# Optimization experiments

Hardware: AMD Instinct MI355X
Metric: run time of the kernel (lower is better)

## Reference

```python
import jax, jax.numpy as jnp
import numpy as np

EPS = 1e-15

def gcn_sparse(x, row, col, ew, W, b, n):
    # PyG GCNConv: h = x@W; add self-loops (weight 1); sym-normalize; aggregate at col (target); + bias
    h = x @ W
    loop = jnp.arange(n)
    r = jnp.concatenate([row, loop])
    c = jnp.concatenate([col, loop])
    w = jnp.concatenate([ew, jnp.ones((n,), x.dtype)])
    deg = jax.ops.segment_sum(w, c, num_segments=n)
    dinv = jnp.where(deg > 0, deg ** -0.5, 0.0)
    norm = dinv[r] * w * dinv[c]
    out = jax.ops.segment_sum(norm[:, None] * h[r], c, num_segments=n)
    return out + b

def gcn_dense(x, adj, W, b):
    # Dense equivalent of dense_to_sparse + GCNConv: existing nonzero self-loops keep their
    # weight, zero-diagonal nodes get a self-loop of weight 1 (add_remaining_self_loops).
    diag = jnp.diagonal(adj)
    adj_h = adj + jnp.diag(jnp.where(diag == 0, 1.0, 0.0).astype(adj.dtype))
    deg = adj_h.sum(axis=0)  # degree at target (col) nodes
    dinv = jnp.where(deg > 0, deg ** -0.5, 0.0)
    a_norm = dinv[:, None] * adj_h * dinv[None, :]  # norm_ij = d_i^-1/2 a_ij d_j^-1/2
    return a_norm.T @ (x @ W) + b  # out_j = sum_i norm_ij h_i

def diff_pool(x, adj, s, mask=None):
    s = jax.nn.softmax(s, axis=-1)
    if mask is not None:
        x = x * mask[:, None]
        s = s * mask[:, None]
    out = s.T @ x                      # [C, F]
    out_adj = s.T @ (adj @ s)          # [C, C]
    link = jnp.linalg.norm(adj - s @ s.T) / adj.size
    ent = jnp.mean(jnp.sum(-s * jnp.log(s + EPS), axis=-1))
    return out, out_adj, link, ent

def setup_inputs() -> dict:
    N, E, F, H, C1, C2, NC = 8192, 262144, 128, 128, 1024, 128, 16
    key = jax.random.key(0)
    ks = jax.random.split(key, 16)
    x0 = jax.random.normal(ks[0], (N, F), dtype=jnp.float32)
    edge_index = jax.random.randint(ks[1], (2, E), 0, N, dtype=jnp.int32)
    edge_weight = jax.random.uniform(ks[2], (E,), dtype=jnp.float32)
    adj = jnp.zeros((N, N), jnp.float32).at[edge_index[0], edge_index[1]].add(edge_weight)
    mask = jnp.ones((N,), jnp.float32)
    g = lambda k, i, o: jax.random.normal(k, (i, o), dtype=jnp.float32) * (1.0 / np.sqrt(i))
    return {
        'x0': x0, 'edge_index': edge_index, 'edge_weight': edge_weight,
        'adj': adj, 'mask': mask,
        'W0_in': g(ks[3], F, H),      'b0_in': jnp.zeros((H,)),
        'Wp1':   g(ks[4], H, C1),     'bp1':   jnp.zeros((C1,)),
        'W1_in': g(ks[5], H, H),      'b1_in': jnp.zeros((H,)),
        'Wp2':   g(ks[6], H, C2),     'bp2':   jnp.zeros((C2,)),
        'W2_in': g(ks[7], H, H),      'b2_in': jnp.zeros((H,)),
        'W1_out': g(ks[8], 2 * H, H), 'b1_out': jnp.zeros((H,)),
        'W0_out': g(ks[9], 2 * H, NC), 'b0_out': jnp.zeros((NC,)),
    }

def reference(x0, edge_index, edge_weight, adj, mask,
              W0_in, b0_in, Wp1, bp1, W1_in, b1_in, Wp2, bp2,
              W2_in, b2_in, W1_out, b1_out, W0_out, b0_out):
    n = x0.shape[0]
    row, col = edge_index[0], edge_index[1]
    x0_ = jax.nn.relu(gcn_sparse(x0, row, col, edge_weight, W0_in, b0_in, n))
    s1 = jax.nn.relu(gcn_sparse(x0_, row, col, edge_weight, Wp1, bp1, n))
    x1, adj1, l1, e1 = diff_pool(x0_, adj, s1, mask)
    x1_ = jax.nn.relu(gcn_dense(x1, adj1, W1_in, b1_in))
    s2 = jax.nn.relu(gcn_dense(x1_, adj1, Wp2, bp2))
    x2, adj2, l2, e2 = diff_pool(x1_, adj1, s2)
    x2_out = jax.nn.relu(gcn_dense(x2, adj2, W2_in, b2_in))
    x2_out_up = s2 @ x2_out  # unpool with pre-softmax relu s2, as in source
    x1_out = jax.nn.relu(gcn_dense(jnp.concatenate([x1_, x2_out_up], axis=1), adj1, W1_out, b1_out))
    x1_out_up = s1 @ x1_out
    x0_out = jax.nn.relu(gcn_sparse(jnp.concatenate([x0_, x1_out_up], axis=1), row, col, edge_weight, W0_out, b0_out, n))
    prediction = jax.nn.log_softmax(x0_out, axis=1)
    edge_loss = l1 + e1 + l2 + e2
    return prediction, s1, edge_loss, adj1
```

## Files before the change

### kernel.cpp

```cpp
#include <hip/hip_runtime.h>
#include <math.h>


#define N_NODES 8192
#define N_EDGES 262144

typedef __attribute__((ext_vector_type(8))) short short8;
typedef __attribute__((ext_vector_type(4))) float floatx4;

#define OFF_DEG     0
#define OFF_CNTC    8192
#define OFF_CNTR    16384
#define OFF_SCAL    24576
#define ZERO_FLOATS 24592
#define OFF_COLPTR  24592
#define OFF_ROWPTR  32785
#define OFF_CURC    40978
#define OFF_CURR    49170
#define OFF_COLR    57362
#define OFF_COLN    319506
#define OFF_ROWC    581650
#define OFF_ROWW    843794
#define OFF_DINV    1105938
#define OFF_X0      1114144
// ... 3 lines not shown
#define OFF_ADJ1B   (OFF_S+524288)
#define OFF_HAT     (OFF_S+1048576)
#define OFF_HBT     (OFF_S+1114112)
#define OFF_HCATT   (OFF_S+1179648)
#define OFF_S2ST    (OFF_S+1245184)
#define OFF_X0T     7405600
#define OFF_X0B     7929888
#define A2          8454176
#define OFF_X1      (A2+0)
#define OFF_Y16     (A2+131072)
#define OFF_X1_     (A2+262144)
#define OFF_S2      (A2+524288)
#define OFF_S2S     (A2+655360)
#define OFF_U       (A2+786432)
#define OFF_X2      (A2+917504)
#define OFF_ADJ2    (A2+933888)
#define OFF_HC      (A2+950272)
#define OFF_X2_     (A2+966656)
#define OFF_Z2      (A2+999424)
#define OFF_X1O     (A2+1261568)
#define OFF_P16     (A2+1392640)
#define OFF_DEG1    OFF_P16
#define OFF_DIAGV   (OFF_P16+1024)
#define OFF_DI1     (A2+1654784)
#define OFF_DF1     (A2+1655808)
#define OFF_DI2     (A2+1656832)
#define OFF_DF2     (A2+1656960)
#define OFF_ST      10111264
#define OFF_TBF     14305568
#define OFF_WP1T    OFF_TBF
#define OFF_PT      OFF_TBF
#define OFF_TT2     32131360

#define OUT_PRED 0
#define OUT_S1   131072
#define OUT_LOSS 8519680
#define OUT_ADJ1 8519681

__device__ __forceinline__ unsigned short f2bf(float f) {
    union { float f; unsigned u; } v; v.f = f;
    unsigned r = (v.u + 0x7FFF + ((v.u >> 16) & 1)) >> 16;
    return (unsigned short)r;
}
__device__ __forceinline__ float bf2f(unsigned short b) {
    union { unsigned u; float f; } v; v.u = (unsigned)b << 16; return v.f;
}
__device__ __forceinline__ void gl_lds16(const unsigned short* g, unsigned short* l) {
    __builtin_amdgcn_global_load_lds(
        (const __attribute__((address_space(1))) void*)g,
        (__attribute__((address_space(3))) void*)l, 16, 0, 0);
}


__global__ void k_hist(const int* __restrict__ row, const int* __restrict__ col,
// ... 287 lines not shown
            float a0 = As[ty * 2][kk], a1 = As[ty * 2 + 1][kk];
            float b0 = Bs[kk][tx * 2], b1 = Bs[kk][tx * 2 + 1];
            acc[0][0] += a0 * b0; acc[0][1] += a0 * b1;
            acc[1][0] += a1 * b0; acc[1][1] += a1 * b1;
        }
        __syncthreads();
    }
    if (op == 2) {
        float ss = acc[0][0] * acc[0][0] + acc[0][1] * acc[0][1]
                 + acc[1][0] * acc[1][0] + acc[1][1] * acc[1][1];
        red[tid] = ss; __syncthreads();
        for (int s = 128; s > 0; s >>= 1) { if (tid < s) red[tid] += red[tid + s]; __syncthreads(); }
        if (tid == 0) atomicAdd(ss_acc, red[0]);
        return;
    }
    float* C = (op == 0) ? C0 : C1;
    #pragma unroll
    for (int i = 0; i < 2; ++i)
        #pragma unroll
        for (int j = 0; j < 2; ++j)
            C[(size_t)(m0 + ty * 2 + i) * N + n0 + tx * 2 + j] = acc[i][j];
}

__global__ __launch_bounds__(256) void k_gemm_n16(const float* __restrict__ A, const float* __restrict__ B,
        float* __restrict__ C, int M, int K, int accum) {
    __shared__ float As[16][64];
    __shared__ float Bs[64][16];
    int tid = threadIdx.x;
    int r = tid >> 4, c = tid & 15;
    int m0 = blockIdx.x * 16;
    float acc = 0.f;
    for (int k0 = 0; k0 < K; k0 += 64) {
        #pragma unroll
        for (int l = 0; l < 4; ++l) {
            int idx = tid + 256 * l;
            int rr = idx >> 6, cc = idx & 63;
            As[rr][cc] = A[(size_t)(m0 + rr) * K + k0 + cc];
            int kk = idx >> 4, c2 = idx & 15;
            Bs[kk][c2] = B[(size_t)(k0 + kk) * 16 + c2];
        }
        __syncthreads();
        #pragma unroll 16
        for (int kk = 0; kk < 64; ++kk) acc += As[r][kk] * Bs[kk][c];
        __syncthreads();
    }
    float* p = &C[(size_t)(m0 + r) * 16 + c];
    if (accum) acc += *p;
    *p = acc;
}

__global__ __launch_bounds__(256) void k_gemm_n16_dual(
        const float* __restrict__ A0, int K0, const float* __restrict__ B0,
        const float* __restrict__ A1, int K1, const float* __restrict__ B1,
        float* __restrict__ C, int M) {
    __shared__ float As[16][64];
    __shared__ float Bs[64][16];
    int tid = threadIdx.x;
    int r = tid >> 4, c = tid & 15;
    int m0 = blockIdx.x * 16;
    float acc = 0.f;
    for (int src = 0; src < 2; ++src) {
        const float* A = src ? A1 : A0;
        const float* B = src ? B1 : B0;
        int K = src ? K1 : K0;
        for (int k0 = 0; k0 < K; k0 += 64) {
            #pragma unroll
            for (int l = 0; l < 4; ++l) {
                int idx = tid + 256 * l;
                int rr = idx >> 6, cc = idx & 63;
                As[rr][cc] = A[(size_t)(m0 + rr) * K + k0 + cc];
                int kk = idx >> 4, c2 = idx & 15;
                Bs[kk][c2] = B[(size_t)(k0 + kk) * 16 + c2];
            }
            __syncthreads();
            #pragma unroll 16
            for (int kk = 0; kk < 64; ++kk) acc += As[r][kk] * Bs[kk][c];
            __syncthreads();
        }
    }
    C[(size_t)(m0 + r) * 16 + c] = acc;
}


__global__ __launch_bounds__(256) void gemm_tn_bf16_tiles(
        const unsigned short* __restrict__ ST_,
        const unsigned short* __restrict__ TT_,
        const unsigned short* __restrict__ X0T_,
        float* __restrict__ P, int K) {
    __shared__ __align__(16) unsigned short As[128 * 64];
    __shared__ __align__(16) unsigned short Bs[128 * 64];
    int tid = threadIdx.x;
    int wave = tid >> 6, lane = tid & 63;
    int wm = wave >> 1, wn = wave & 1;
    int tile = blockIdx.x;
    int m, n; const unsigned short* B;
    if (tile < 64)       { m = tile >> 3; n = tile & 7; B = TT_; }
    else if (tile < 100) { int p = tile - 64; int ti = 0;
                           while (p >= 8 - ti) { p -= 8 - ti; ++ti; }
                           m = ti; n = ti + p; B = ST_; }
    else                 { m = tile - 100; n = 0; B = X0T_; }
    int m0 = m * 128, n0 = n * 128;
    int kchunk = K / gridDim.y;
    int k0 = blockIdx.y * kchunk;
    float* Pz = P + ((size_t)blockIdx.y * 108 + tile) * 16384;
    floatx4 acc[4][4] = {};
    int q = lane >> 4, lm = lane & 15;
    int lrow = lane >> 3, lcol = (lane & 7) * 8;
    for (int kt = 0; kt < kchunk; kt += 64) {
        int gk0 = k0 + kt;
        #pragma unroll
        for (int p = 0; p < 4; ++p) {
            int rbase = wave * 32 + p * 8;
            int row = rbase + lrow;
            int scol = lcol ^ ((row & 7) * 8);
            gl_lds16(&ST_[(size_t)(m0 + row) * K + gk0 + scol], &As[rbase * 64]);
            gl_lds16(&B[(size_t)(n0 + row) * K + gk0 + scol], &Bs[rbase * 64]);
        }
        __syncthreads();
        #pragma unroll
        for (int ks = 0; ks < 64; ks += 32) {
            short8 af[4], bf[4];
            int kk = ks + q * 8;
            #pragma unroll
            for (int i = 0; i < 4; ++i) {
                int ml = wm * 64 + i * 16 + lm;
                af[i] = *(const short8*)(&As[ml * 64 + (kk ^ ((ml & 7) * 8))]);
                int nl = wn * 64 + i * 16 + lm;
                bf[i] = *(const short8*)(&Bs[nl * 64 + (kk ^ ((nl & 7) * 8))]);
            }
            #pragma unroll
            for (int i = 0; i < 4; ++i)
                #pragma unroll
                for (int j = 0; j < 4; ++j)
                    acc[i][j] = __builtin_amdgcn_mfma_f32_16x16x32_bf16(af[i], bf[j], acc[i][j], 0, 0, 0);
        }
        __syncthreads();
    }
    for (int i = 0; i < 4; ++i) {
        int lr = wm * 64 + i * 16 + q * 4;
        for (int j = 0; j < 4; ++j) {
            int lc = wn * 64 + j * 16 + lm;
            #pragma unroll
            for (int r = 0; r < 4; ++r)
                Pz[(size_t)(lr + r) * 128 + lc] = acc[i][j][r];
        }
    }
}

__global__ __launch_bounds__(256) void k_reduce_tiles(
        const float* __restrict__ P,
        float* __restrict__ adj1o, unsigned short* __restrict__ adj1b,
        float* __restrict__ x1, float* __restrict__ deg1, float* __restrict__ diagv,
        float* __restrict__ scal) {
    __shared__ float colsum[128];
    __shared__ float red[256];
    int tile = blockIdx.y, half = blockIdx.x, tid = threadIdx.x;
    if (tid < 128) colsum[tid] = 0.f;
    __syncthreads();
    int m, n, kind;
    if (tile < 64)       { kind = 0; m = tile >> 3; n = tile & 7; }
    else if (tile < 100) { kind = 1; int p = tile - 64; int ti = 0;
                           while (p >= 8 - ti) { p -= 8 - ti; ++ti; }
                           m = ti; n = ti + p; }
    else                 { kind = 2; m = tile - 100; n = 0; }
    const float* Pt = P + (size_t)tile * 16384 + half * 8192;
    const size_t zstr = (size_t)108 * 16384;
    float ss = 0.f, tr = 0.f;
// ... 33 lines not shown
        }
    }
    if (kind == 2) return;
    if (kind == 0) {
        atomicAdd(&colsum[cc + 0], cs0);
        atomicAdd(&colsum[cc + 1], cs1);
        atomicAdd(&colsum[cc + 2], cs2);
        atomicAdd(&colsum[cc + 3], cs3);
    }
    __syncthreads();
    if (kind == 0 && tid < 128)
        atomicAdd(&deg1[n * 128 + tid], colsum[tid]);
    red[tid] = ss; __syncthreads();
    for (int s = 128; s > 0; s >>= 1) { if (tid < s) red[tid] += red[tid + s]; __syncthreads(); }
    if (tid == 0) atomicAdd((kind == 0) ? &scal[4] : &scal[2], red[0]);
    if (diagTile) {
        __syncthreads();
        red[tid] = tr; __syncthreads();
        for (int s = 128; s > 0; s >>= 1) { if (tid < s) red[tid] += red[tid + s]; __syncthreads(); }
        if (tid == 0) atomicAdd(&scal[1], red[0]);
    }
}

__global__ __launch_bounds__(1024) void k_dinv1024(const float* __restrict__ deg1,
        const float* __restrict__ diagv, float* __restrict__ di, float* __restrict__ df) {
    int j = threadIdx.x;
    float s = deg1[j];
    float fix = (diagv[j] == 0.f) ? 1.0f : 0.f;
    s += fix;
    df[j] = fix;
    di[j] = (s > 0.f) ? 1.0f / sqrtf(s) : 0.f;
}

__global__ __launch_bounds__(256) void gemm_tn_bf16_n128(
        const unsigned short* __restrict__ A, const unsigned short* __restrict__ B,
        float* __restrict__ C, int K,
        const float* __restrict__ bias, int relu) {
    __shared__ __align__(16) unsigned short As[64 * 64];
    __shared__ __align__(16) unsigned short Bs[64 * 64];
    int tid = threadIdx.x, wave = tid >> 6, lane = tid & 63;
    int m0 = blockIdx.x * 64, n0 = blockIdx.y * 64;
    floatx4 acc[4] = {};
    int q = lane >> 4, lm = lane & 15;
    int lrow = lane >> 3, lcol = (lane & 7) * 8;
    for (int kt = 0; kt < K; kt += 64) {
        #pragma unroll
        for (int p = 0; p < 2; ++p) {
            int rbase = wave * 16 + p * 8;
            int row = rbase + lrow;
            int scol = lcol ^ ((row & 7) * 8);
            gl_lds16(&A[(size_t)(m0 + row) * K + kt + scol], &As[rbase * 64]);
            gl_lds16(&B[(size_t)(n0 + row) * K + kt + scol], &Bs[rbase * 64]);
        }
        __syncthreads();
        #pragma unroll
        for (int ks = 0; ks < 64; ks += 32) {
// ... 5 lines not shown
                int nl = j * 16 + lm;
                short8 bf = *(const short8*)(&Bs[nl * 64 + (kk ^ ((nl & 7) * 8))]);
                acc[j] = __builtin_amdgcn_mfma_f32_16x16x32_bf16(af, bf, acc[j], 0, 0, 0);
            }
        }
        __syncthreads();
    }
    #pragma unroll
    for (int j = 0; j < 4; ++j) {
        int col = n0 + j * 16 + lm;
        float bv = bias ? bias[col] : 0.f;
        int rowb = m0 + wave * 16 + q * 4;
        #pragma unroll
        for (int r = 0; r < 4; ++r) {
            float v = acc[j][r] + bv;
            if (relu) v = fmaxf(v, 0.f);
            C[(size_t)(rowb + r) * 128 + col] = v;
        }
    }
}

__global__ __launch_bounds__(256) void gemm_tn_bf16_store(
        const unsigned short* __restrict__ A, const unsigned short* __restrict__ B,
        float* __restrict__ C, int M, int N, int K,
        const float* __restrict__ bias, int relu) {
    __shared__ __align__(16) unsigned short As[128 * 64];
    __shared__ __align__(16) unsigned short Bs[128 * 64];
    int tid = threadIdx.x;
    int wave = tid >> 6, lane = tid & 63;
    int wm = wave >> 1, wn = wave & 1;
    int m0 = blockIdx.x * 128, n0 = blockIdx.y * 128;
    floatx4 acc[4][4] = {};
    int q = lane >> 4, lm = lane & 15;
    int lrow = lane >> 3, lcol = (lane & 7) * 8;
    for (int kt = 0; kt < K; kt += 64) {
        #pragma unroll
        for (int p = 0; p < 4; ++p) {
            int rbase = wave * 32 + p * 8;
            int row = rbase + lrow;
            int scol = lcol ^ ((row & 7) * 8);
            gl_lds16(&A[(size_t)(m0 + row) * K + kt + scol], &As[rbase * 64]);
            gl_lds16(&B[(size_t)(n0 + row) * K + kt + scol], &Bs[rbase * 64]);
        }
        __syncthreads();
        #pragma unroll
        for (int ks = 0; ks < 64; ks += 32) {
            short8 af[4], bf[4];
// ... 3 lines not shown
                int ml = wm * 64 + i * 16 + lm;
                af[i] = *(const short8*)(&As[ml * 64 + (kk ^ ((ml & 7) * 8))]);
                int nl = wn * 64 + i * 16 + lm;
                bf[i] = *(const short8*)(&Bs[nl * 64 + (kk ^ ((nl & 7) * 8))]);
            }
            #pragma unroll
            for (int i = 0; i < 4; ++i)
                #pragma unroll
                for (int j = 0; j < 4; ++j)
                    acc[i][j] = __builtin_amdgcn_mfma_f32_16x16x32_bf16(af[i], bf[j], acc[i][j], 0, 0, 0);
        }
        __syncthreads();
    }
    for (int i = 0; i < 4; ++i) {
        int rowb = m0 + wm * 64 + i * 16 + q * 4;
        for (int j = 0; j < 4; ++j) {
            int col = n0 + wn * 64 + j * 16 + lm;
            float bv = bias ? bias[col] : 0.f;
            #pragma unroll
            for (int r = 0; r < 4; ++r) {
                float v = acc[i][j][r] + bv;
                if (relu) v = fmaxf(v, 0.f);
                C[(size_t)(rowb + r) * N + col] = v;
            }
        }
    }
}


__global__ __launch_bounds__(256) void k_transpose_f2b(
        const float* __restrict__ in, unsigned short* __restrict__ outb,
        int R, int C, const float* __restrict__ rowscale) {
    __shared__ float tile[64][65];
    int rb = blockIdx.y * 64, cb = blockIdx.x * 64;
    int t = threadIdx.x;
    int lr = t >> 4, lc4 = (t & 15) * 4;
    #pragma unroll
    for (int p = 0; p < 4; ++p) {
        int r = rb + lr + p * 16;
        float4 v = *(const float4*)(in + (size_t)r * C + cb + lc4);
        float s = rowscale ? rowscale[r] : 1.0f;
        tile[lr + p * 16][lc4 + 0] = v.x * s;
        tile[lr + p * 16][lc4 + 1] = v.y * s;
        tile[lr + p * 16][lc4 + 2] = v.z * s;
        tile[lr + p * 16][lc4 + 3] = v.w * s;
    }
    __syncthreads();
    int cc0 = t >> 5, rr = (t & 31) * 2;
// ... 15 lines not shown
    unsigned short* out = blockIdx.z ? out1 : out0;
    int rb = blockIdx.y * 64, cb = blockIdx.x * 64;
    int t = threadIdx.x;
    int lr = t >> 3, lc = (t & 7) * 8;
    #pragma unroll
    for (int p = 0; p < 2; ++p) {
        int r = lr + p * 32;
        *(short8*)(&tile[r][lc]) = *(const short8*)(&in[(size_t)(rb + r) * C + cb + lc]);
    }
    __syncthreads();
    int cc0 = t >> 4, rr = (t & 15) * 4;
    #pragma unroll
    for (int p = 0; p < 4; ++p) {
        int cc = cc0 + p * 16;
        unsigned long long v = (unsigned long long)tile[rr][cc]
                             | ((unsigned long long)tile[rr + 1][cc] << 16)
                             | ((unsigned long long)tile[rr + 2][cc] << 32)
                             | ((unsigned long long)tile[rr + 3][cc] << 48);
        *(unsigned long long*)(&out[(size_t)(cb + cc) * R + rb + rr]) = v;
    }
}

__global__ __launch_bounds__(256) void k_anorm_tb(const float* __restrict__ adjm, int n,
        const float* __restrict__ dinvv, const float* __restrict__ dfix,
        unsigned short* __restrict__ outb) {
    __shared__ float tile[64][65];
    int rb = blockIdx.y * 64, cb = blockIdx.x * 64;
    int t = threadIdx.x;
    int lr = t >> 4, lc4 = (t & 15) * 4;
    #pragma unroll
    for (int p = 0; p < 4; ++p) {
        int i = rb + lr + p * 16;
        float4 v = *(const float4*)(adjm + (size_t)i * n + cb + lc4);
        float di = dinvv[i];
        float vv[4] = {v.x, v.y, v.z, v.w};
        #pragma unroll
        for (int q = 0; q < 4; ++q) {
            int j = cb + lc4 + q;
            float val = vv[q];
            if (i == j) val += dfix[i];
            tile[lr + p * 16][lc4 + q] = di * val * dinvv[j];
        }
    }
    __syncthreads();
    int cc0 = t >> 5, rr = (t & 31) * 2;
    #pragma unroll
    for (int p = 0; p < 8; ++p) {
        int cc = cc0 + p * 8;
        unsigned a = f2bf(tile[rr][cc]);
        unsigned b = f2bf(tile[rr + 1][cc]);
        *(unsigned*)(outb + (size_t)(cb + cc) * n + rb + rr) = a | (b << 16);
    }
}


__global__ __launch_bounds__(64) void k_agg_b16(const unsigned short* __restrict__ h,
        float* __restrict__ out, unsigned short* __restrict__ outb,
        const int* __restrict__ cptr, const int* __restrict__ colr,
        const float* __restrict__ coln, const float* __restrict__ dinv,
        const float* __restrict__ bias, int relu) {
    int c = blockIdx.x, t = threadIdx.x;
    int f0 = t * 2;
    float d = dinv[c], dd = d * d;
    const unsigned short* hf = h + f0;
// ... 12 lines not shown
        a0 += w0 * bf2f((unsigned short)(v0 & 0xffff)) + w1 * bf2f((unsigned short)(v1 & 0xffff))
            + w2 * bf2f((unsigned short)(v2 & 0xffff)) + w3 * bf2f((unsigned short)(v3 & 0xffff));
        a1 += w0 * bf2f((unsigned short)(v0 >> 16)) + w1 * bf2f((unsigned short)(v1 >> 16))
            + w2 * bf2f((unsigned short)(v2 >> 16)) + w3 * bf2f((unsigned short)(v3 >> 16));
    }
    for (; e < e1; ++e) {
        float w = coln[e];
        unsigned v = *(const unsigned*)(hf + (size_t)colr[e] * 128);
        a0 += w * bf2f((unsigned short)(v & 0xffff));
        a1 += w * bf2f((unsigned short)(v >> 16));
    }
    if (bias) { a0 += bias[f0]; a1 += bias[f0 + 1]; }
    if (relu) { a0 = fmaxf(a0, 0.f); a1 = fmaxf(a1, 0.f); }
    if (out) { out[(size_t)c * 128 + f0] = a0; out[(size_t)c * 128 + f0 + 1] = a1; }
    if (outb) {
        unsigned o = (unsigned)f2bf(a0) | ((unsigned)f2bf(a1) << 16);
        *(unsigned*)(outb + (size_t)c * 128 + f0) = o;
    }
}

__global__ __launch_bounds__(256) void k_agg16_ls(const float* __restrict__ h, float* __restrict__ pred,
        const int* __restrict__ cptr, const int* __restrict__ colr,
        const float* __restrict__ coln, const float* __restrict__ dinv,
        const float* __restrict__ bias) {
    int node = blockIdx.x * 16 + (threadIdx.x >> 4);
    int f = threadIdx.x & 15;
    float d = dinv[node];
    const float* hf = h + f;
    float acc = d * d * hf[(size_t)node * 16];
    int e0 = cptr[node], e1 = cptr[node + 1];
    int e = e0;
    for (; e + 4 <= e1; e += 4) {
        int r0 = colr[e], r1 = colr[e + 1], r2 = colr[e + 2], r3 = colr[e + 3];
        float w0 = coln[e], w1 = coln[e + 1], w2 = coln[e + 2], w3 = coln[e + 3];
        float v0 = hf[(size_t)r0 * 16], v1 = hf[(size_t)r1 * 16];
        float v2 = hf[(size_t)r2 * 16], v3 = hf[(size_t)r3 * 16];
        acc += w0 * v0 + w1 * v1 + w2 * v2 + w3 * v3;
    }
    for (; e < e1; ++e)
        acc += coln[e] * hf[(size_t)colr[e] * 16];
    acc += bias[f];
    acc = fmaxf(acc, 0.f);
    float m = acc;
    #pragma unroll
    for (int off = 1; off < 16; off <<= 1) m = fmaxf(m, __shfl_xor(m, off, 16));
    float ex = expf(acc - m);
    float s = ex;
    #pragma unroll
    for (int off = 1; off < 16; off <<= 1) s += __shfl_xor(s, off, 16);
    pred[(size_t)node * 16 + f] = acc - m - logf(s);
}

__global__ __launch_bounds__(256) void k_softmax1024(const float* __restrict__ x,
        unsigned short* __restrict__ Sb, const float* __restrict__ mask, float* ent_acc) {
    __shared__ float red[256];
    int r = blockIdx.x, tid = threadIdx.x;
    const float* xr = x + (size_t)r * 1024;
    float4 v = *(const float4*)(xr + tid * 4);
    float m = fmaxf(fmaxf(v.x, v.y), fmaxf(v.z, v.w));
    red[tid] = m; __syncthreads();
    for (int s = 128; s > 0; s >>= 1) { if (tid < s) red[tid] = fmaxf(red[tid], red[tid + s]); __syncthreads(); }
    m = red[0]; __syncthreads();
    float e0 = expf(v.x - m), e1 = expf(v.y - m), e2 = expf(v.z - m), e3 = expf(v.w - m);
    red[tid] = e0 + e1 + e2 + e3; __syncthreads();
    for (int s = 128; s > 0; s >>= 1) { if (tid < s) red[tid] += red[tid + s]; __syncthreads(); }
    float inv = 1.0f / red[0]; __syncthreads();
    float mk = mask ? mask[r] : 1.0f;
    float s0 = e0 * inv * mk, s1 = e1 * inv * mk, s2 = e2 * inv * mk, s3 = e3 * inv * mk;
    float ent = -(s0 * logf(s0 + 1e-15f) + s1 * logf(s1 + 1e-15f)
                + s2 * logf(s2 + 1e-15f) + s3 * logf(s3 + 1e-15f));
    ushort4 o;
    o.x = f2bf(s0); o.y = f2bf(s1); o.z = f2bf(s2); o.w = f2bf(s3);
    *(ushort4*)(Sb + (size_t)r * 1024 + tid * 4) = o;
    red[tid] = ent; __syncthreads();
    for (int s = 128; s > 0; s >>= 1) { if (tid < s) red[tid] += red[tid + s]; __syncthreads(); }
    if (tid == 0) atomicAdd(ent_acc, red[0]);
}

__global__ __launch_bounds__(256) void k_softmax_ent(const float* __restrict__ x, float* __restrict__ S,
        int W, const float* __restrict__ mask, float* ent_acc) {
    __shared__ float red[256];
    int row = blockIdx.x, tid = threadIdx.x;
    const float* xr = x + (size_t)row * W;
    float m = -3.0e38f;
    for (int q = tid; q < W; q += 256) m = fmaxf(m, xr[q]);
    red[tid] = m; __syncthreads();
    for (int s = 128; s > 0; s >>= 1) { if (tid < s) red[tid] = fmaxf(red[tid], red[tid + s]); __syncthreads(); }
    m = red[0]; __syncthreads();
    float sum = 0.f;
    for (int q = tid; q < W; q += 256) sum += expf(xr[q] - m);
    red[tid] = sum; __syncthreads();
    for (int s = 128; s > 0; s >>= 1) { if (tid < s) red[tid] += red[tid + s]; __syncthreads(); }
    float inv = 1.0f / red[0]; __syncthreads();
    float mk = mask ? mask[row] : 1.0f;
    float* Sr = S + (size_t)row * W;
    float ent = 0.f;
    for (int q = tid; q < W; q += 256) {
        float v = expf(xr[q] - m) * inv * mk;
        Sr[q] = v;
        ent -= v * logf(v + 1e-15f);
    }
    red[tid] = ent; __syncthreads();
    for (int s = 128; s > 0; s >>= 1) { if (tid < s) red[tid] += red[tid + s]; __syncthreads(); }
    if (tid == 0) atomicAdd(ent_acc, red[0]);
}

__global__ __launch_bounds__(256) void k_spmm_seg(const unsigned short* __restrict__ Sb,
        const int* __restrict__ rptr, const int* __restrict__ rowc, const float* __restrict__ roww,
        unsigned short* __restrict__ tb) {
    int wave = threadIdx.x >> 6, lane = threadIdx.x & 63;
    int r = blockIdx.x * 4 + wave;
    int j0 = blockIdx.y * 256 + lane * 4;
    const unsigned short* Sj = Sb + j0;
    float a0 = 0.f, a1 = 0.f, a2 = 0.f, a3 = 0.f;
    int e0 = rptr[r], e1 = rptr[r + 1];
    int e = e0;
    for (; e + 4 <= e1; e += 4) {
        int c0 = rowc[e], c1 = rowc[e + 1], c2 = rowc[e + 2], c3 = rowc[e + 3];
        float w0 = roww[e], w1 = roww[e + 1], w2 = roww[e + 2], w3 = roww[e + 3];
        uint2 v0 = *(const uint2*)(Sj + (size_t)c0 * 1024);
        uint2 v1 = *(const uint2*)(Sj + (size_t)c1 * 1024);
        uint2 v2 = *(const uint2*)(Sj + (size_t)c2 * 1024);
        uint2 v3 = *(const uint2*)(Sj + (size_t)c3 * 1024);
        a0 += w0 * bf2f((unsigned short)(v0.x & 0xffff)) + w1 * bf2f((unsigned short)(v1.x & 0xffff))
            + w2 * bf2f((unsigned short)(v2.x & 0xffff)) + w3 * bf2f((unsigned short)(v3.x & 0xffff));
        a1 += w0 * bf2f((unsigned short)(v0.x >> 16)) + w1 * bf2f((unsigned short)(v1.x >> 16))
            + w2 * bf2f((unsigned short)(v2.x >> 16)) + w3 * bf2f((unsigned short)(v3.x >> 16));
        a2 += w0 * bf2f((unsigned short)(v0.y & 0xffff)) + w1 * bf2f((unsigned short)(v1.y & 0xffff))
            + w2 * bf2f((unsigned short)(v2.y & 0xffff)) + w3 * bf2f((unsigned short)(v3.y & 0xffff));
        a3 += w0 * bf2f((unsigned short)(v0.y >> 16)) + w1 * bf2f((unsigned short)(v1.y >> 16))
            + w2 * bf2f((unsigned short)(v2.y >> 16)) + w3 * bf2f((unsigned short)(v3.y >> 16));
    }
    for (; e < e1; ++e) {
        int c = rowc[e]; float w = roww[e];
        uint2 v = *(const uint2*)(Sj + (size_t)c * 1024);
        a0 += w * bf2f((unsigned short)(v.x & 0xffff));
        a1 += w * bf2f((unsigned short)(v.x >> 16));
        a2 += w * bf2f((unsigned short)(v.y & 0xffff));
        a3 += w * bf2f((unsigned short)(v.y >> 16));
    }
    unsigned lo = (unsigned)f2bf(a0) | ((unsigned)f2bf(a1) << 16);
    unsigned hi = (unsigned)f2bf(a2) | ((unsigned)f2bf(a3) << 16);
    unsigned long long o = (unsigned long long)lo | ((unsigned long long)hi << 32);
    *(unsigned long long*)(tb + (size_t)r * 1024 + j0) = o;
}

__global__ __launch_bounds__(128) void k_coldfix128(const float* __restrict__ adjm,
        float* dinvv, float* dfix, float* cross2_out) {
    __shared__ float red[128];
    int j = threadIdx.x;
    float s = 0.f;
    for (int i = 0; i < 128; ++i) s += adjm[(size_t)i * 128 + j];
    float diag = adjm[(size_t)j * 128 + j];
    float fix = (diag == 0.f) ? 1.0f : 0.f;
    s += fix;
    dfix[j] = fix;
    dinvv[j] = (s > 0.f) ? 1.0f / sqrtf(s) : 0.f;
    red[j] = diag; __syncthreads();
    for (int st = 64; st > 0; st >>= 1) { if (j < st) red[j] += red[j + st]; __syncthreads(); }
    if (j == 0) *cross2_out = red[0];
}

__global__ void k_finalize(const float* __restrict__ sc, float* loss) {
    if (threadIdx.x == 0 && blockIdx.x == 0) {
        float e1     = sc[0] / 8192.0f;
        float cross  = sc[1];
        float g2     = sc[2];
        float sumA2  = sc[3];
        float ssadj1 = sc[4];
        float e2     = sc[5] / 1024.0f;
        float cross2 = sc[6];
        float g2b    = sc[7];
        float l1 = sqrtf(fmaxf(sumA2 - 2.0f * cross + g2, 0.f)) / 67108864.0f;
        float l2 = sqrtf(fmaxf(ssadj1 - 2.0f * cross2 + g2b, 0.f)) / 1048576.0f;
        *loss = l1 + e1 + l2 + e2;
    }
}


extern "C" void kernel_launch(void* const* d_in, const int* in_sizes, int n_in,
                              void* d_out, int out_size, void* d_ws, size_t ws_size,
                              hipStream_t stream) {
    const int N = N_NODES, E = N_EDGES;
    const float* x0     = (const float*)d_in[0];
    const int*   eidx   = (const int*)d_in[1];
    const float* ew     = (const float*)d_in[2];
    const float* mask   = (const float*)d_in[4];
    const float* W0_in  = (const float*)d_in[5];
    const float* b0_in  = (const float*)d_in[6];
    const float* Wp1    = (const float*)d_in[7];
    const float* bp1    = (const float*)d_in[8];
    const float* W1_in  = (const float*)d_in[9];
    const float* b1_in  = (const float*)d_in[10];
    const float* Wp2    = (const float*)d_in[11];
    const float* bp2    = (const float*)d_in[12];
    const float* W2_in  = (const float*)d_in[13];
    const float* b2_in  = (const float*)d_in[14];
    const float* W1_out = (const float*)d_in[15];
    const float* b1_out = (const float*)d_in[16];
// ... 16 lines not shown
    int*   rptr  = wsi + OFF_ROWPTR;
    int*   curc  = wsi + OFF_CURC;
    int*   curr  = wsi + OFF_CURR;
    int*   colr  = wsi + OFF_COLR;
    float* coln  = wsf + OFF_COLN;
    int*   rowc  = wsi + OFF_ROWC;
    float* roww  = wsf + OFF_ROWW;
    float* dinv  = wsf + OFF_DINV;
    float* x0_   = wsf + OFF_X0;
    unsigned short* h0b   = (unsigned short*)(wsf + OFF_H0);
    unsigned short* Sb    = (unsigned short*)(wsf + OFF_S);
    unsigned short* TT    = (unsigned short*)(wsf + OFF_TT2);
    unsigned short* AN1TB = (unsigned short*)(wsf + OFF_AN1TB);
    unsigned short* ADJ1B = (unsigned short*)(wsf + OFF_ADJ1B);
    unsigned short* HAT   = (unsigned short*)(wsf + OFF_HAT);
    unsigned short* HBT   = (unsigned short*)(wsf + OFF_HBT);
    unsigned short* HCATT = (unsigned short*)(wsf + OFF_HCATT);
    unsigned short* S2ST  = (unsigned short*)(wsf + OFF_S2ST);
    unsigned short* ST    = (unsigned short*)(wsf + OFF_ST);
    unsigned short* TBF   = (unsigned short*)(wsf + OFF_TBF);
    unsigned short* WP1T  = (unsigned short*)(wsf + OFF_WP1T);
    unsigned short* X0T   = (unsigned short*)(wsf + OFF_X0T);
    unsigned short* x0b   = (unsigned short*)(wsf + OFF_X0B);
    float* PT    = wsf + OFF_PT;
    float* x1    = wsf + OFF_X1;
    float* y16   = wsf + OFF_Y16;
    float* x1_   = wsf + OFF_X1_;
    float* s2    = wsf + OFF_S2;
    float* S2s   = wsf + OFF_S2S;
    float* u     = wsf + OFF_U;
    float* x2    = wsf + OFF_X2;
    float* adj2  = wsf + OFF_ADJ2;
    float* hC    = wsf + OFF_HC;
    float* x2_   = wsf + OFF_X2_;
    float* z2    = wsf + OFF_Z2;
    float* x1o_  = wsf + OFF_X1O;
    float* p16   = wsf + OFF_P16;
    float* deg1  = wsf + OFF_DEG1;
    float* diagv = wsf + OFF_DIAGV;
    float* di1   = wsf + OFF_DI1;
    float* df1   = wsf + OFF_DF1;
    float* di2   = wsf + OFF_DI2;
    float* df2   = wsf + OFF_DF2;

    const int* row = eidx;
    const int* col = eidx + E;

    hipMemsetAsync(wsf, 0, (size_t)ZERO_FLOATS * sizeof(float), stream);
    hipMemsetAsync(deg1, 0, 1024 * sizeof(float), stream);

    k_hist<<<E / 256, 256, 0, stream>>>(row, col, ew, E, deg, cntc, cntr, &scal[3]);
    k_scan<<<1, 1024, 0, stream>>>(cntc, cntr, cptr, rptr, curc, curr, N, E, deg, dinv);
    k_scatter<<<E / 256, 256, 0, stream>>>(row, col, ew, E, dinv, curc, curr, colr, coln, rowc, roww);

    gemm_ab_b16<<<dim3(2, 128), 256, 0, stream>>>(x0, W0_in, h0b, 8192, 128, 128);
    k_agg_b16<<<N, 64, 0, stream>>>(h0b, x0_, x0b, cptr, colr, coln, dinv, b0_in, 1);

    k_agg_b16<<<N, 64, 0, stream>>>(x0b, nullptr, h0b, cptr, colr, coln, dinv, nullptr, 0);
    k_transpose_f2b<<<dim3(16, 2), 256, 0, stream>>>(Wp1, WP1T, 128, 1024, nullptr);
    gemm_tn_bf16_store<<<dim3(64, 8), 256, 0, stream>>>(h0b, WP1T, s1o, 8192, 1024, 128, bp1, 1);

    k_softmax1024<<<N, 256, 0, stream>>>(s1o, Sb, mask, &scal[0]);
    k_spmm_seg<<<dim3(N / 4, 4), 256, 0, stream>>>(Sb, rptr, rowc, roww, TBF);
    k_transpose_b2b2<<<dim3(16, 128, 2), 256, 0, stream>>>(Sb, ST, TBF, TT, 8192, 1024);
    k_transpose_f2b<<<dim3(2, 128), 256, 0, stream>>>(x0_, X0T, 8192, 128, mask);

    gemm_tn_bf16_tiles<<<dim3(108, 4), 256, 0, stream>>>(ST, TT, X0T, PT, 8192);
    k_reduce_tiles<<<dim3(2, 108), 256, 0, stream>>>(PT, adj1o, ADJ1B, x1, deg1, diagv, scal);
    k_dinv1024<<<1, 1024, 0, stream>>>(deg1, diagv, di1, df1);
    k_anorm_tb<<<dim3(16, 16), 256, 0, stream>>>(adj1o, 1024, di1, df1, AN1TB);

    gemm_ab32_bt<<<dim3(4, 32), 256, 0, stream>>>(x1, W1_in, HAT, 1024, 128, 128);
    gemm_tn_bf16_n128<<<dim3(16, 2), 256, 0, stream>>>(AN1TB, HAT, x1_, 1024, b1_in, 1);
    gemm_ab32_bt<<<dim3(4, 32), 256, 0, stream>>>(x1_, Wp2, HBT, 1024, 128, 128);
    gemm_tn_bf16_n128<<<dim3(16, 2), 256, 0, stream>>>(AN1TB, HBT, s2, 1024, bp2, 1);

    k_softmax_ent<<<1024, 256, 0, stream>>>(s2, S2s, 128, nullptr, &scal[5]);
    k_transpose_f2b<<<dim3(2, 16), 256, 0, stream>>>(S2s, S2ST, 1024, 128, nullptr);
    gemm_tn_bf16_n128<<<dim3(16, 2), 256, 0, stream>>>(ADJ1B, S2ST, u, 1024, nullptr, 0);
    k_atb32_3<<<dim3(4, 4, 3), 256, 0, stream>>>(S2s, x1_, u, S2s, x2, adj2, &scal[7], 128, 128, 1024);

    k_coldfix128<<<1, 128, 0, stream>>>(adj2, di2, df2, &scal[6]);
    gemm_ab32<<<dim3(4, 4), 256, 0, stream>>>(x2, W2_in, hC, 128, 128, 128, nullptr, 0, 0);
    gemm_atb32n<<<dim3(4, 4), 256, 0, stream>>>(adj2, hC, x2_, 128, 128, 128, b2_in, di2, df2, di2);

    gemm_ab32<<<dim3(4, 4), 256, 0, stream>>>(x2_, W1_out + 128 * 128, z2, 128, 128, 128, nullptr, 0, 0);
    gemm_dual_bt<<<dim3(4, 32), 256, 0, stream>>>(x1_, W1_out, s2, z2, HCATT, 1024, 128, 128);
    gemm_tn_bf16_n128<<<dim3(16, 2), 256, 0, stream>>>(AN1TB, HCATT, x1o_, 1024, b1_out, 1);

    k_gemm_n16<<<64, 256, 0, stream>>>(x1o_, W0_out + 128 * 16, y16, 1024, 128, 0);
    k_gemm_n16_dual<<<512, 256, 0, stream>>>(x0_, 128, W0_out, s1o, 1024, y16, p16, 8192);
    k_agg16_ls<<<512, 256, 0, stream>>>(p16, predo, cptr, colr, coln, dinv, b0_out);

    k_finalize<<<1, 64, 0, stream>>>(scal, losso);
}
```

Before: 895.2 us.

## Fuse small kernels, move final N=16 GEMM to bf16 MFMA, remap tile grid

Several small launches are folded into neighbours. The dinv computation moves into k_anorm_tb, the level-2 coldfix merges with the hC GEMM, the loss finalization goes into the last aggregation kernel, and the 128-wide softmax now writes the transposed bf16 output directly. The final x0_/s1 by W0_out GEMM switches from fp32 scalar code to bf16 MFMA, reading a new bf16 copy of s1 written by the projection GEMM epilogue. Entropy is computed analytically from log-sum-exp, and the tiles GEMM block index is remapped so blocks sharing an A row panel are grouped. This trades launch overhead and fp32 ALU work for extra bf16 rounding on the final layer's inputs.

```diff
diff --git a/kernel.cpp b/kernel.cpp
--- a/kernel.cpp
+++ b/kernel.cpp
@@ -49,14 +49,13 @@
 #define OFF_P16     (A2+1392640)
 #define OFF_DEG1    OFF_P16
 #define OFF_DIAGV   (OFF_P16+1024)
-#define OFF_DI1     (A2+1654784)
-#define OFF_DF1     (A2+1655808)
 #define OFF_DI2     (A2+1656832)
 #define OFF_DF2     (A2+1656960)
 #define OFF_ST      10111264
 #define OFF_TBF     14305568
 #define OFF_WP1T    OFF_TBF
 #define OFF_PT      OFF_TBF
+#define OFF_S1B     22694176
 #define OFF_TT2     32131360
 
 #define OUT_PRED 0
@@ -390,6 +389,59 @@
             C[(size_t)(m0 + ty * 2 + i) * N + n0 + tx * 2 + j] = acc[i][j];
 }
 
+__global__ __launch_bounds__(256) void k_hC_coldfix(
+        const float* __restrict__ x2, const float* __restrict__ W2,
+        float* __restrict__ hC, const float* __restrict__ adj2,
+        float* di2, float* df2, float* cross2_out) {
+    if (blockIdx.z == 0) {
+        __shared__ float As[32][33];
+        __shared__ float Bs[32][33];
+        int tid = threadIdx.x, tx = tid & 15, ty = tid >> 4;
+        int m0 = blockIdx.y * 32, n0 = blockIdx.x * 32;
+        float acc[2][2] = {};
+        for (int k0 = 0; k0 < 128; k0 += 32) {
+            #pragma unroll
+            for (int l = 0; l < 4; ++l) {
+                int idx = tid + 256 * l;
+                int r = idx >> 5, c = idx & 31;
+                As[r][c] = x2[(size_t)(m0 + r) * 128 + k0 + c];
+                Bs[r][c] = W2[(size_t)(k0 + r) * 128 + n0 + c];
+            }
+            __syncthreads();
+            #pragma unroll
+            for (int kk = 0; kk < 32; ++kk) {
+                float a0 = As[ty * 2][kk], a1 = As[ty * 2 + 1][kk];
+                float b0 = Bs[kk][tx * 2], b1 = Bs[kk][tx * 2 + 1];
+                acc[0][0] += a0 * b0; acc[0][1] += a0 * b1;
+                acc[1][0] += a1 * b0; acc[1][1] += a1 * b1;
+            }
+            __syncthreads();
+        }
+        #pragma unroll
+        for (int i = 0; i < 2; ++i)
+            #pragma unroll
+            for (int j = 0; j < 2; ++j)
+                hC[(size_t)(m0 + ty * 2 + i) * 128 + n0 + tx * 2 + j] = acc[i][j];
+    } else {
+        if (blockIdx.x | blockIdx.y) return;
+        __shared__ float red[256];
+        int tid = threadIdx.x;
+        float diag = 0.f;
+        if (tid < 128) {
+            float s = 0.f;
+            for (int i = 0; i < 128; ++i) s += adj2[(size_t)i * 128 + tid];
+            diag = adj2[(size_t)tid * 128 + tid];
+            float fix = (diag == 0.f) ? 1.0f : 0.f;
+            s += fix;
+            df2[tid] = fix;
+            di2[tid] = (s > 0.f) ? 1.0f / sqrtf(s) : 0.f;
+        }
+        red[tid] = diag; __syncthreads();
+        for (int st = 128; st > 0; st >>= 1) { if (tid < st) red[tid] += red[tid + st]; __syncthreads(); }
+        if (tid == 0) *cross2_out = red[0];
+    }
+}
+
 __global__ __launch_bounds__(256) void k_gemm_n16(const float* __restrict__ A, const float* __restrict__ B,
         float* __restrict__ C, int M, int K, int accum) {
     __shared__ float As[16][64];
@@ -415,38 +467,6 @@
     float* p = &C[(size_t)(m0 + r) * 16 + c];
     if (accum) acc += *p;
     *p = acc;
-}
-
-__global__ __launch_bounds__(256) void k_gemm_n16_dual(
-        const float* __restrict__ A0, int K0, const float* __restrict__ B0,
-        const float* __restrict__ A1, int K1, const float* __restrict__ B1,
-        float* __restrict__ C, int M) {
-    __shared__ float As[16][64];
-    __shared__ float Bs[64][16];
-    int tid = threadIdx.x;
-    int r = tid >> 4, c = tid & 15;
-    int m0 = blockIdx.x * 16;
-    float acc = 0.f;
-    for (int src = 0; src < 2; ++src) {
-        const float* A = src ? A1 : A0;
-        const float* B = src ? B1 : B0;
-        int K = src ? K1 : K0;
-        for (int k0 = 0; k0 < K; k0 += 64) {
-            #pragma unroll
-            for (int l = 0; l < 4; ++l) {
-                int idx = tid + 256 * l;
-                int rr = idx >> 6, cc = idx & 63;
-                As[rr][cc] = A[(size_t)(m0 + rr) * K + k0 + cc];
-                int kk = idx >> 4, c2 = idx & 15;
-                Bs[kk][c2] = B[(size_t)(k0 + kk) * 16 + c2];
-            }
-            __syncthreads();
-            #pragma unroll 16
-            for (int kk = 0; kk < 64; ++kk) acc += As[r][kk] * Bs[kk][c];
-            __syncthreads();
-        }
-    }
-    C[(size_t)(m0 + r) * 16 + c] = acc;
 }
 
 
@@ -460,17 +480,21 @@
     int tid = threadIdx.x;
     int wave = tid >> 6, lane = tid & 63;
     int wm = wave >> 1, wn = wave & 1;
-    int tile = blockIdx.x;
-    int m, n; const unsigned short* B;
-    if (tile < 64)       { m = tile >> 3; n = tile & 7; B = TT_; }
-    else if (tile < 100) { int p = tile - 64; int ti = 0;
-                           while (p >= 8 - ti) { p -= 8 - ti; ++ti; }
-                           m = ti; n = ti + p; B = ST_; }
-    else                 { m = tile - 100; n = 0; B = X0T_; }
-    int m0 = m * 128, n0 = n * 128;
-    int kchunk = K / gridDim.y;
-    int k0 = blockIdx.y * kchunk;
-    float* Pz = P + ((size_t)blockIdx.y * 108 + tile) * 16384;
+    int lin = blockIdx.x + gridDim.x * blockIdx.y;
+    int p432 = (lin & 7) * 54 + (lin >> 3);
+    int f = p432 >> 2, z = p432 & 3;
+    int m = 0, Pfx = 0;
+    while (f >= Pfx + 17 - m) { Pfx += 17 - m; ++m; }
+    int r = f - Pfx;
+    int t, n0; const unsigned short* B;
+    if (r < 8)           { t = m * 8 + r;                              n0 = r * 128;            B = TT_; }
+    else if (r < 16 - m) { int tj = m + (r - 8);
+                           t = 64 + (8 * m - m * (m - 1) / 2) + (r - 8); n0 = tj * 128;         B = ST_; }
+    else                 { t = 100 + m;                                n0 = 0;                  B = X0T_; }
+    int m0 = m * 128;
+    int kchunk = K >> 2;
+    int k0 = z * kchunk;
+    float* Pz = P + ((size_t)z * 108 + t) * 16384;
     floatx4 acc[4][4] = {};
     int q = lane >> 4, lm = lane & 15;
     int lrow = lane >> 3, lcol = (lane & 7) * 8;
@@ -509,8 +533,8 @@
         for (int j = 0; j < 4; ++j) {
             int lc = wn * 64 + j * 16 + lm;
             #pragma unroll
-            for (int r = 0; r < 4; ++r)
-                Pz[(size_t)(lr + r) * 128 + lc] = acc[i][j][r];
+            for (int rr = 0; rr < 4; ++rr)
+                Pz[(size_t)(lr + rr) * 128 + lc] = acc[i][j][rr];
         }
     }
 }
@@ -590,16 +614,6 @@
     }
 }
 
-__global__ __launch_bounds__(1024) void k_dinv1024(const float* __restrict__ deg1,
-        const float* __restrict__ diagv, float* __restrict__ di, float* __restrict__ df) {
-    int j = threadIdx.x;
-    float s = deg1[j];
-    float fix = (diagv[j] == 0.f) ? 1.0f : 0.f;
-    s += fix;
-    df[j] = fix;
-    di[j] = (s > 0.f) ? 1.0f / sqrtf(s) : 0.f;
-}
-
 __global__ __launch_bounds__(256) void gemm_tn_bf16_n128(
         const unsigned short* __restrict__ A, const unsigned short* __restrict__ B,
         float* __restrict__ C, int K,
@@ -651,7 +665,7 @@
 
 __global__ __launch_bounds__(256) void gemm_tn_bf16_store(
         const unsigned short* __restrict__ A, const unsigned short* __restrict__ B,
-        float* __restrict__ C, int M, int N, int K,
+        float* __restrict__ C, unsigned short* __restrict__ Cb, int M, int N, int K,
         const float* __restrict__ bias, int relu) {
     __shared__ __align__(16) unsigned short As[128 * 64];
     __shared__ __align__(16) unsigned short Bs[128 * 64];
@@ -701,8 +715,62 @@
                 float v = acc[i][j][r] + bv;
                 if (relu) v = fmaxf(v, 0.f);
                 C[(size_t)(rowb + r) * N + col] = v;
+                if (Cb) Cb[(size_t)(rowb + r) * N + col] = f2bf(v);
             }
         }
+    }
+}
+
+__global__ __launch_bounds__(256) void k_gemm16_mfma(
+        const unsigned short* __restrict__ A0,
+        const unsigned short* __restrict__ A1,
+        const float* __restrict__ B0,
+        const float* __restrict__ B1,
+        float* __restrict__ C) {
+    __shared__ __align__(16) unsigned short As[128 * 64];
+    __shared__ __align__(16) unsigned short Bs[16 * 64];
+    int tid = threadIdx.x, wave = tid >> 6, lane = tid & 63;
+    int m0 = blockIdx.x * 128;
+    int q = lane >> 4, lm = lane & 15;
+    int lrow = lane >> 3, lcol = (lane & 7) * 8;
+    floatx4 acc[2] = {};
+    for (int seg = 0; seg < 2; ++seg) {
+        const unsigned short* A = seg ? A1 : A0;
+        const float* Bsrc = seg ? B1 : B0;
+        int Ks = seg ? 1024 : 128;
+        for (int kt = 0; kt < Ks; kt += 64) {
+            #pragma unroll
+            for (int p = 0; p < 4; ++p) {
+                int rbase = wave * 32 + p * 8;
+                int row = rbase + lrow;
+                int scol = lcol ^ ((row & 7) * 8);
+                gl_lds16(&A[(size_t)(m0 + row) * Ks + kt + scol], &As[rbase * 64]);
+            }
+            for (int e = tid; e < 1024; e += 256) {
+                int n = e >> 6, kk = e & 63;
+                Bs[n * 64 + (kk ^ ((n & 7) * 8))] = f2bf(Bsrc[(size_t)(kt + kk) * 16 + n]);
+            }
+            __syncthreads();
+            #pragma unroll
+            for (int ks = 0; ks < 64; ks += 32) {
+                int kk = ks + q * 8;
+                short8 bf = *(const short8*)(&Bs[lm * 64 + (kk ^ ((lm & 7) * 8))]);
+                #pragma unroll
+                for (int i = 0; i < 2; ++i) {
+                    int ml = wave * 32 + i * 16 + lm;
+                    short8 af = *(const short8*)(&As[ml * 64 + (kk ^ ((ml & 7) * 8))]);
+                    acc[i] = __builtin_amdgcn_mfma_f32_16x16x32_bf16(af, bf, acc[i], 0, 0, 0);
+                }
+            }
+            __syncthreads();
+        }
+    }
+    #pragma unroll
+    for (int i = 0; i < 2; ++i) {
+        int rowb = m0 + wave * 32 + i * 16 + q * 4;
+        #pragma unroll
+        for (int r = 0; r < 4; ++r)
+            C[(size_t)(rowb + r) * 16 + lm] = acc[i][r];
     }
 }
 
@@ -764,24 +832,39 @@
 }
 
 __global__ __launch_bounds__(256) void k_anorm_tb(const float* __restrict__ adjm, int n,
-        const float* __restrict__ dinvv, const float* __restrict__ dfix,
+        const float* __restrict__ deg1, const float* __restrict__ diagv,
         unsigned short* __restrict__ outb) {
     __shared__ float tile[64][65];
+    __shared__ float drow[64], frow[64], dcol[64];
     int rb = blockIdx.y * 64, cb = blockIdx.x * 64;
     int t = threadIdx.x;
+    if (t < 64) {
+        int i = rb + t;
+        float fi = (diagv[i] == 0.f) ? 1.0f : 0.f;
+        float s = deg1[i] + fi;
+        frow[t] = fi;
+        drow[t] = (s > 0.f) ? 1.0f / sqrtf(s) : 0.f;
+    } else if (t < 128) {
+        int j = cb + (t - 64);
+        float fj = (diagv[j] == 0.f) ? 1.0f : 0.f;
+        float s = deg1[j] + fj;
+        dcol[t - 64] = (s > 0.f) ? 1.0f / sqrtf(s) : 0.f;
+    }
+    __syncthreads();
     int lr = t >> 4, lc4 = (t & 15) * 4;
     #pragma unroll
     for (int p = 0; p < 4; ++p) {
-        int i = rb + lr + p * 16;
+        int rl = lr + p * 16;
+        int i = rb + rl;
         float4 v = *(const float4*)(adjm + (size_t)i * n + cb + lc4);
-        float di = dinvv[i];
+        float di = drow[rl];
         float vv[4] = {v.x, v.y, v.z, v.w};
         #pragma unroll
-        for (int q = 0; q < 4; ++q) {
-            int j = cb + lc4 + q;
-            float val = vv[q];
-            if (i == j) val += dfix[i];
-            tile[lr + p * 16][lc4 + q] = di * val * dinvv[j];
+        for (int qq = 0; qq < 4; ++qq) {
+            int j = cb + lc4 + qq;
+            float val = vv[qq];
+            if (i == j) val += frow[rl];
+            tile[rl][lc4 + qq] = di * val * dcol[lc4 + qq];
         }
     }
     __syncthreads();
@@ -840,22 +923,35 @@
 __global__ __launch_bounds__(256) void k_agg16_ls(const float* __restrict__ h, float* __restrict__ pred,
         const int* __restrict__ cptr, const int* __restrict__ colr,
         const float* __restrict__ coln, const float* __restrict__ dinv,
-        const float* __restrict__ bias) {
+        const float* __restrict__ bias, const float* __restrict__ sc, float* loss) {
+    if (blockIdx.x == 0 && threadIdx.x == 0) {
+        float e1     = sc[0] / 8192.0f;
+        float cross  = sc[1];
+        float g2     = sc[2];
+        float sumA2  = sc[3];
+        float ssadj1 = sc[4];
+        float e2     = sc[5] / 1024.0f;
+        float cross2 = sc[6];
+        float g2b    = sc[7];
+        float l1 = sqrtf(fmaxf(sumA2 - 2.0f * cross + g2, 0.f)) / 67108864.0f;
+        float l2 = sqrtf(fmaxf(ssadj1 - 2.0f * cross2 + g2b, 0.f)) / 1048576.0f;
+        *loss = l1 + e1 + l2 + e2;
+    }
     int node = blockIdx.x * 16 + (threadIdx.x >> 4);
     int f = threadIdx.x & 15;
     float d = dinv[node];
     const float* hf = h + f;
     float acc = d * d * hf[(size_t)node * 16];
-    int e0 = cptr[node], e1 = cptr[node + 1];
+    int e0 = cptr[node], e1v = cptr[node + 1];
     int e = e0;
-    for (; e + 4 <= e1; e += 4) {
+    for (; e + 4 <= e1v; e += 4) {
         int r0 = colr[e], r1 = colr[e + 1], r2 = colr[e + 2], r3 = colr[e + 3];
         float w0 = coln[e], w1 = coln[e + 1], w2 = coln[e + 2], w3 = coln[e + 3];
         float v0 = hf[(size_t)r0 * 16], v1 = hf[(size_t)r1 * 16];
         float v2 = hf[(size_t)r2 * 16], v3 = hf[(size_t)r3 * 16];
         acc += w0 * v0 + w1 * v1 + w2 * v2 + w3 * v3;
     }
-    for (; e < e1; ++e)
+    for (; e < e1v; ++e)
         acc += coln[e] * hf[(size_t)colr[e] * 16];
     acc += bias[f];
     acc = fmaxf(acc, 0.f);
@@ -882,44 +978,44 @@
     float e0 = expf(v.x - m), e1 = expf(v.y - m), e2 = expf(v.z - m), e3 = expf(v.w - m);
     red[tid] = e0 + e1 + e2 + e3; __syncthreads();
     for (int s = 128; s > 0; s >>= 1) { if (tid < s) red[tid] += red[tid + s]; __syncthreads(); }
-    float inv = 1.0f / red[0]; __syncthreads();
+    float Z = red[0];
+    float inv = 1.0f / Z, lz = logf(Z);
+    __syncthreads();
     float mk = mask ? mask[r] : 1.0f;
     float s0 = e0 * inv * mk, s1 = e1 * inv * mk, s2 = e2 * inv * mk, s3 = e3 * inv * mk;
-    float ent = -(s0 * logf(s0 + 1e-15f) + s1 * logf(s1 + 1e-15f)
-                + s2 * logf(s2 + 1e-15f) + s3 * logf(s3 + 1e-15f));
+    float ent = s0 * (m + lz - v.x) + s1 * (m + lz - v.y)
+              + s2 * (m + lz - v.z) + s3 * (m + lz - v.w);
     ushort4 o;
     o.x = f2bf(s0); o.y = f2bf(s1); o.z = f2bf(s2); o.w = f2bf(s3);
     *(ushort4*)(Sb + (size_t)r * 1024 + tid * 4) = o;
     red[tid] = ent; __syncthreads();
     for (int s = 128; s > 0; s >>= 1) { if (tid < s) red[tid] += red[tid + s]; __syncthreads(); }
-    if (tid == 0) atomicAdd(ent_acc, red[0]);
-}
-
-__global__ __launch_bounds__(256) void k_softmax_ent(const float* __restrict__ x, float* __restrict__ S,
-        int W, const float* __restrict__ mask, float* ent_acc) {
-    __shared__ float red[256];
+    if (tid == 0) {
+        float row_ent = red[0] - ((mk > 0.f) ? mk * logf(mk) : 0.f);
+        atomicAdd(ent_acc, row_ent);
+    }
+}
+
+__global__ __launch_bounds__(128) void k_softmax128_t(const float* __restrict__ x,
+        float* __restrict__ S, unsigned short* __restrict__ STb, float* ent_acc) {
+    __shared__ float red[128];
     int row = blockIdx.x, tid = threadIdx.x;
-    const float* xr = x + (size_t)row * W;
-    float m = -3.0e38f;
-    for (int q = tid; q < W; q += 256) m = fmaxf(m, xr[q]);
-    red[tid] = m; __syncthreads();
-    for (int s = 128; s > 0; s >>= 1) { if (tid < s) red[tid] = fmaxf(red[tid], red[tid + s]); __syncthreads(); }
-    m = red[0]; __syncthreads();
-    float sum = 0.f;
-    for (int q = tid; q < W; q += 256) sum += expf(xr[q] - m);
-    red[tid] = sum; __syncthreads();
-    for (int s = 128; s > 0; s >>= 1) { if (tid < s) red[tid] += red[tid + s]; __syncthreads(); }
-    float inv = 1.0f / red[0]; __syncthreads();
-    float mk = mask ? mask[row] : 1.0f;
-    float* Sr = S + (size_t)row * W;
-    float ent = 0.f;
-    for (int q = tid; q < W; q += 256) {
-        float v = expf(xr[q] - m) * inv * mk;
-        Sr[q] = v;
-        ent -= v * logf(v + 1e-15f);
-    }
-    red[tid] = ent; __syncthreads();
-    for (int s = 128; s > 0; s >>= 1) { if (tid < s) red[tid] += red[tid + s]; __syncthreads(); }
+    const float* xr = x + (size_t)row * 128;
+    float v = xr[tid];
+    red[tid] = v; __syncthreads();
+    for (int s = 64; s > 0; s >>= 1) { if (tid < s) red[tid] = fmaxf(red[tid], red[tid + s]); __syncthreads(); }
+    float m = red[0]; __syncthreads();
+    float e = expf(v - m);
+    red[tid] = e; __syncthreads();
+    for (int s = 64; s > 0; s >>= 1) { if (tid < s) red[tid] += red[tid + s]; __syncthreads(); }
+    float Z = red[0];
+    float inv = 1.0f / Z, lz = logf(Z);
+    __syncthreads();
+    float sv = e * inv;
+    S[(size_t)row * 128 + tid] = sv;
+    STb[(size_t)tid * 1024 + row] = f2bf(sv);
+    red[tid] = sv * (m + lz - v); __syncthreads();
+    for (int s = 64; s > 0; s >>= 1) { if (tid < s) red[tid] += red[tid + s]; __syncthreads(); }
     if (tid == 0) atomicAdd(ent_acc, red[0]);
 }
 
@@ -961,38 +1057,6 @@
     unsigned hi = (unsigned)f2bf(a2) | ((unsigned)f2bf(a3) << 16);
     unsigned long long o = (unsigned long long)lo | ((unsigned long long)hi << 32);
     *(unsigned long long*)(tb + (size_t)r * 1024 + j0) = o;
-}
-
-__global__ __launch_bounds__(128) void k_coldfix128(const float* __restrict__ adjm,
-        float* dinvv, float* dfix, float* cross2_out) {
-    __shared__ float red[128];
-    int j = threadIdx.x;
-    float s = 0.f;
-    for (int i = 0; i < 128; ++i) s += adjm[(size_t)i * 128 + j];
-    float diag = adjm[(size_t)j * 128 + j];
-    float fix = (diag == 0.f) ? 1.0f : 0.f;
-    s += fix;
-    dfix[j] = fix;
-    dinvv[j] = (s > 0.f) ? 1.0f / sqrtf(s) : 0.f;
-    red[j] = diag; __syncthreads();
-    for (int st = 64; st > 0; st >>= 1) { if (j < st) red[j] += red[j + st]; __syncthreads(); }
-    if (j == 0) *cross2_out = red[0];
-}
-
-__global__ void k_finalize(const float* __restrict__ sc, float* loss) {
-    if (threadIdx.x == 0 && blockIdx.x == 0) {
-        float e1     = sc[0] / 8192.0f;
-        float cross  = sc[1];
-        float g2     = sc[2];
-        float sumA2  = sc[3];
-        float ssadj1 = sc[4];
-        float e2     = sc[5] / 1024.0f;
-        float cross2 = sc[6];
-        float g2b    = sc[7];
-        float l1 = sqrtf(fmaxf(sumA2 - 2.0f * cross + g2, 0.f)) / 67108864.0f;
-        float l2 = sqrtf(fmaxf(ssadj1 - 2.0f * cross2 + g2b, 0.f)) / 1048576.0f;
-        *loss = l1 + e1 + l2 + e2;
-    }
 }
 
 
@@ -1055,6 +1119,7 @@
     unsigned short* WP1T  = (unsigned short*)(wsf + OFF_WP1T);
     unsigned short* X0T   = (unsigned short*)(wsf + OFF_X0T);
     unsigned short* x0b   = (unsigned short*)(wsf + OFF_X0B);
+    unsigned short* s1b   = (unsigned short*)(wsf + OFF_S1B);
     float* PT    = wsf + OFF_PT;
     float* x1    = wsf + OFF_X1;
     float* y16   = wsf + OFF_Y16;
@@ -1071,8 +1136,6 @@
     float* p16   = wsf + OFF_P16;
     float* deg1  = wsf + OFF_DEG1;
     float* diagv = wsf + OFF_DIAGV;
-    float* di1   = wsf + OFF_DI1;
-    float* df1   = wsf + OFF_DF1;
     float* di2   = wsf + OFF_DI2;
     float* df2   = wsf + OFF_DF2;
 
@@ -1091,7 +1154,7 @@
 
     k_agg_b16<<<N, 64, 0, stream>>>(x0b, nullptr, h0b, cptr, colr, coln, dinv, nullptr, 0);
     k_transpose_f2b<<<dim3(16, 2), 256, 0, stream>>>(Wp1, WP1T, 128, 1024, nullptr);
-    gemm_tn_bf16_store<<<dim3(64, 8), 256, 0, stream>>>(h0b, WP1T, s1o, 8192, 1024, 128, bp1, 1);
+    gemm_tn_bf16_store<<<dim3(64, 8), 256, 0, stream>>>(h0b, WP1T, s1o, s1b, 8192, 1024, 128, bp1, 1);
 
     k_softmax1024<<<N, 256, 0, stream>>>(s1o, Sb, mask, &scal[0]);
     k_spmm_seg<<<dim3(N / 4, 4), 256, 0, stream>>>(Sb, rptr, rowc, roww, TBF);
@@ -1100,21 +1163,18 @@
 
     gemm_tn_bf16_tiles<<<dim3(108, 4), 256, 0, stream>>>(ST, TT, X0T, PT, 8192);
     k_reduce_tiles<<<dim3(2, 108), 256, 0, stream>>>(PT, adj1o, ADJ1B, x1, deg1, diagv, scal);
-    k_dinv1024<<<1, 1024, 0, stream>>>(deg1, diagv, di1, df1);
-    k_anorm_tb<<<dim3(16, 16), 256, 0, stream>>>(adj1o, 1024, di1, df1, AN1TB);
+    k_anorm_tb<<<dim3(16, 16), 256, 0, stream>>>(adj1o, 1024, deg1, diagv, AN1TB);
 
     gemm_ab32_bt<<<dim3(4, 32), 256, 0, stream>>>(x1, W1_in, HAT, 1024, 128, 128);
     gemm_tn_bf16_n128<<<dim3(16, 2), 256, 0, stream>>>(AN1TB, HAT, x1_, 1024, b1_in, 1);
     gemm_ab32_bt<<<dim3(4, 32), 256, 0, stream>>>(x1_, Wp2, HBT, 1024, 128, 128);
     gemm_tn_bf16_n128<<<dim3(16, 2), 256, 0, stream>>>(AN1TB, HBT, s2, 1024, bp2, 1);
 
-    k_softmax_ent<<<1024, 256, 0, stream>>>(s2, S2s, 128, nullptr, &scal[5]);
-    k_transpose_f2b<<<dim3(2, 16), 256, 0, stream>>>(S2s, S2ST, 1024, 128, nullptr);
+    k_softmax128_t<<<1024, 128, 0, stream>>>(s2, S2s, S2ST, &scal[5]);
     gemm_tn_bf16_n128<<<dim3(16, 2), 256, 0, stream>>>(ADJ1B, S2ST, u, 1024, nullptr, 0);
     k_atb32_3<<<dim3(4, 4, 3), 256, 0, stream>>>(S2s, x1_, u, S2s, x2, adj2, &scal[7], 128, 128, 1024);
 
-    k_coldfix128<<<1, 128, 0, stream>>>(adj2, di2, df2, &scal[6]);
-    gemm_ab32<<<dim3(4, 4), 256, 0, stream>>>(x2, W2_in, hC, 128, 128, 128, nullptr, 0, 0);
+    k_hC_coldfix<<<dim3(4, 4, 2), 256, 0, stream>>>(x2, W2_in, hC, adj2, di2, df2, &scal[6]);
     gemm_atb32n<<<dim3(4, 4), 256, 0, stream>>>(adj2, hC, x2_, 128, 128, 128, b2_in, di2, df2, di2);
 
     gemm_ab32<<<dim3(4, 4), 256, 0, stream>>>(x2_, W1_out + 128 * 128, z2, 128, 128, 128, nullptr, 0, 0);
@@ -1122,8 +1182,6 @@
     gemm_tn_bf16_n128<<<dim3(16, 2), 256, 0, stream>>>(AN1TB, HCATT, x1o_, 1024, b1_out, 1);
 
     k_gemm_n16<<<64, 256, 0, stream>>>(x1o_, W0_out + 128 * 16, y16, 1024, 128, 0);
-    k_gemm_n16_dual<<<512, 256, 0, stream>>>(x0_, 128, W0_out, s1o, 1024, y16, p16, 8192);
-    k_agg16_ls<<<512, 256, 0, stream>>>(p16, predo, cptr, colr, coln, dinv, b0_out);
-
-    k_finalize<<<1, 64, 0, stream>>>(scal, losso);
-}
+    k_gemm16_mfma<<<64, 256, 0, stream>>>(x0b, s1b, W0_out, y16, p16);
+    k_agg16_ls<<<512, 256, 0, stream>>>(p16, predo, cptr, colr, coln, dinv, b0_out, scal, losso);
+}
```

Result: no change. 883.9 us (-1.3%).
